# Optimization experiments

Measured on AMD Instinct MI355X. Metric: run time of the kernel, lower is better.

The kernel has to match this reference:

```python
import jax, jax.numpy as jnp
import numpy as np

N = 50000      # nodes
E = 800000     # edges (avg degree 16)
IN, HID, OUT = 256, 128, 64


def _glorot(key, shape):
    fan_in, fan_out = shape[0], shape[1]
    limit = np.sqrt(6.0 / (fan_in + fan_out))
    return jax.random.uniform(key, shape, jnp.float32, -limit, limit)


def setup_inputs() -> dict:
    key = jax.random.key(0)
    ks = jax.random.split(key, 8)
    x = jax.random.normal(ks[0], (N, IN), jnp.float32)
    edge_index = jax.random.randint(ks[1], (2, E), 0, N, dtype=jnp.int64)
    W1 = _glorot(ks[2], (IN, HID))
    b1 = jnp.zeros((HID,), jnp.float32)
    W2 = _glorot(ks[3], (HID, OUT))
    b2 = jnp.zeros((OUT,), jnp.float32)
    aw1 = _glorot(ks[4], (HID, 1))
    ab1 = jnp.zeros((1,), jnp.float32)
    aw2 = _glorot(ks[5], (OUT, 1))
    ab2 = jnp.zeros((1,), jnp.float32)
    return {"x": x, "edge_index": edge_index, "W1": W1, "b1": b1,
            "W2": W2, "b2": b2, "aw1": aw1, "ab1": ab1, "aw2": aw2, "ab2": ab2}


def gcn_conv(x, W, b, src, dst, n):
    # PyG GCNConv: add self-loops, symmetric degree normalization, then aggregate.
    h = x @ W                                   # [n, out]
    loops = jnp.arange(n, dtype=src.dtype)
    s = jnp.concatenate([src, loops])           # [E+n]
    d = jnp.concatenate([dst, loops])
    deg = jax.ops.segment_sum(jnp.ones(s.shape[0], h.dtype), d, num_segments=n)
    dinv = jnp.where(deg > 0, jax.lax.rsqrt(deg), 0.0)
    norm = dinv[s] * dinv[d]                    # [E+n]
    out = jax.ops.segment_sum(h[s] * norm[:, None], d, num_segments=n)
    return out + b


def reference(x, edge_index, W1, b1, W2, b2, aw1, ab1, aw2, ab2):
    # eval mode: dropout is identity
    src, dst = edge_index[0], edge_index[1]
    h = gcn_conv(x, W1, b1, src, dst, N)
    h = jax.nn.relu(h)
    h = h * jax.nn.sigmoid(h @ aw1 + ab1)       # sigmoid attention gate 1
    h = gcn_conv(h, W2, b2, src, dst, N)
    return h * jax.nn.sigmoid(h @ aw2 + ab2)    # sigmoid attention gate 2
```

## Files before the change

kernel.cpp:

```cpp
#include <hip/hip_runtime.h>
#include <math.h>

#define N_NODES 50000
#define N_EDGES 800000
#define D_IN    256
#define D_HID   128
#define D_OUT   64

#define NB 196
#define CH 4096

typedef unsigned int u32;
typedef unsigned short u16;
typedef __attribute__((ext_vector_type(8))) short bf16x8;
typedef __attribute__((ext_vector_type(4))) float f32x4;

__device__ __forceinline__ float bflo(u32 u) {
    union { u32 i; float f; } c; c.i = u << 16; return c.f;
}
__device__ __forceinline__ float bfhi(u32 u) {
    union { u32 i; float f; } c; c.i = u & 0xffff0000u; return c.f;
}
__device__ __forceinline__ u32 pack_bf2(float a, float b) {
    union { float f; u32 i; } ca, cb; ca.f = a; cb.f = b;
    u32 ra = (ca.i + 0x7fffu + ((ca.i >> 16) & 1u)) >> 16;
    u32 rb = (cb.i + 0x7fffu + ((cb.i >> 16) & 1u)) & 0xffff0000u;
    return ra | rb;
}
__device__ __forceinline__ u32 bf16_rne(float f) {
    union { float f; u32 i; } c; c.f = f;
    return (c.i + 0x7fffu + ((c.i >> 16) & 1u)) >> 16;
}
__device__ __forceinline__ float bfbits_to_f32(u32 hb) {
    union { u32 i; float f; } c; c.i = hb << 16; return c.f;
}

__global__ void k_detect(const void* __restrict__ ei, int* __restrict__ flag) {
    int t = threadIdx.x;
    int v = ((const int*)ei)[2 * t + 1];
    if (v != 0) atomicOr(flag, 1);
}

__device__ __forceinline__ int edge_at(const void* ei, int is64, int which, int i) {
    if (is64) return (int)((const long long*)ei)[(size_t)which * N_EDGES + i];
    return ((const int*)ei)[which * N_EDGES + i];
}


__global__ __launch_bounds__(256) void k_hist(const void* __restrict__ ei,
                                              const int* __restrict__ flag,
                                              int* __restrict__ bcnt) {
    __shared__ int h[NB];
    int t = threadIdx.x;
    for (int i = t; i < NB; i += 256) h[i] = 0;
    __syncthreads();
    int is64 = (flag[0] == 0);
    for (int i = blockIdx.x * 256 + t; i < N_EDGES; i += gridDim.x * 256) {
        int d = edge_at(ei, is64, 1, i);
        atomicAdd(&h[d >> 8], 1);
    }
    __syncthreads();
    for (int i = t; i < NB; i += 256) if (h[i]) atomicAdd(&bcnt[i], h[i]);
}

__global__ void k_bscan(const int* __restrict__ bcnt, int* __restrict__ bstart,
                        int* __restrict__ bcur) {
    __shared__ int sm[256];
    int t = threadIdx.x;
    int v = (t < NB) ? bcnt[t] : 0;
    sm[t] = v; __syncthreads();
    for (int off = 1; off < 256; off <<= 1) {
        int a = (t >= off) ? sm[t - off] : 0;
        __syncthreads();
        sm[t] += a;
        __syncthreads();
    }
    if (t < NB) { bstart[t] = sm[t] - v; bcur[t] = sm[t] - v; }
}

__global__ __launch_bounds__(256) void k_scatter1(const void* __restrict__ ei,
                                                  const int* __restrict__ flag,
                                                  int* __restrict__ bcur,
                                                  u32* __restrict__ ebuf) {
    __shared__ int h[NB], gbase[NB], lc[NB];
    int t = threadIdx.x;
    for (int i = t; i < NB; i += 256) { h[i] = 0; lc[i] = 0; }
    __syncthreads();
    int is64 = (flag[0] == 0);
    int base = blockIdx.x * CH;

    u32 p[CH / 256];
    #pragma unroll
    for (int j = 0; j < CH / 256; ++j) {
        int i = base + j * 256 + t;
        if (i < N_EDGES) {
            int s = edge_at(ei, is64, 0, i);
            int d = edge_at(ei, is64, 1, i);
            p[j] = (u32)s | ((u32)d << 16);
            atomicAdd(&h[d >> 8], 1);
        }
    }
    __syncthreads();
    for (int i = t; i < NB; i += 256) if (h[i]) gbase[i] = atomicAdd(&bcur[i], h[i]);
    __syncthreads();
    #pragma unroll
    for (int j = 0; j < CH / 256; ++j) {
        int i = base + j * 256 + t;
        if (i < N_EDGES) {
            int b = (int)(p[j] >> 24);
            int lp = atomicAdd(&lc[b], 1);
            ebuf[gbase[b] + lp] = p[j];
        }
    }
}

__global__ __launch_bounds__(256) void k_scatter2(const u32* __restrict__ ebuf,
                                                  const int* __restrict__ bstart,
                                                  const int* __restrict__ bcnt,
                                                  int* __restrict__ rowstart,
                                                  int* __restrict__ cnt,
                                                  float* __restrict__ dinv,
                                                  int* __restrict__ colidx) {
    __shared__ int h2[256], lofs[256], cur[256], sm[256];
    int b = blockIdx.x, t = threadIdx.x;
    int e0 = bstart[b], ne = bcnt[b];
    h2[t] = 0; cur[t] = 0;
    __syncthreads();
    for (int i = t; i < ne; i += 256) {
        u32 p = ebuf[e0 + i];
        atomicAdd(&h2[(p >> 16) & 255], 1);
    }
    __syncthreads();
    int v = h2[t]; sm[t] = v; __syncthreads();
    for (int off = 1; off < 256; off <<= 1) {
        int a = (t >= off) ? sm[t - off] : 0;
        __syncthreads();
        sm[t] += a;
        __syncthreads();
    }
    lofs[t] = sm[t] - v;
    __syncthreads();
    int node = (b << 8) + t;
    if (node < N_NODES) {
        rowstart[node] = e0 + lofs[t];
        cnt[node] = v;
        dinv[node] = rsqrtf(1.0f + (float)v);
    }
    for (int i = t; i < ne; i += 256) {
        u32 p = ebuf[e0 + i];
        int dl = (p >> 16) & 255;
        int lp = atomicAdd(&cur[dl], 1);
        colidx[e0 + lofs[dl] + lp] = (int)(p & 0xffffu);
    }
}

__global__ void k_wsplit(const float* __restrict__ W, u16* __restrict__ tHi,
                         u16* __restrict__ tLo, int K, int NF) {
    int i = blockIdx.x * 256 + threadIdx.x;
    if (i >= K * NF) return;
    int k = i / NF, c = i - k * NF;
    float f = W[i];
    u32 hb = bf16_rne(f);
    u32 lb = bf16_rne(f - bfbits_to_f32(hb));
    tHi[(size_t)c * K + k] = (u16)hb;
    tLo[(size_t)c * K + k] = (u16)lb;
}

template <int K, int NF>
__global__ __launch_bounds__(256) void k_gemm_mfma(
    const float* __restrict__ A, const u16* __restrict__ tHi,
    const u16* __restrict__ tLo, const float* __restrict__ dinv,
    u32* __restrict__ Cp, int M) {
    constexpr int NT = NF / 16;
    constexpr int LDK = 40;
    __shared__ u16 aH[128][LDK], aL[128][LDK];
    __shared__ u16 wH[NF][LDK], wL[NF][LDK];

    const int t = threadIdx.x;
    const int lane = t & 63, wv = t >> 6;
    const int m0 = blockIdx.x * 128;
    const int lr = lane & 15, lk = (lane >> 4) * 8;

    f32x4 acc[2][NT] = {};

    const int arow = t >> 1;
    const int akq = (t & 1) * 16;
    const bool aok = (m0 + arow) < M;
    const float* asrc = A + (size_t)(m0 + arow) * K + akq;

    for (int ks = 0; ks < K; ks += 32) {
        {
            float buf[16];
            #pragma unroll
            for (int j = 0; j < 16; ++j) buf[j] = 0.0f;
            if (aok) {
                const float4* p = (const float4*)(asrc + ks);
                float4 v0 = p[0], v1 = p[1], v2 = p[2], v3 = p[3];
                buf[0] = v0.x; buf[1] = v0.y; buf[2]  = v0.z; buf[3]  = v0.w;
                buf[4] = v1.x; buf[5] = v1.y; buf[6]  = v1.z; buf[7]  = v1.w;
                buf[8] = v2.x; buf[9] = v2.y; buf[10] = v2.z; buf[11] = v2.w;
                buf[12] = v3.x; buf[13] = v3.y; buf[14] = v3.z; buf[15] = v3.w;
            }
            u32 h[16], l[16];
            #pragma unroll
            for (int j = 0; j < 16; ++j) {
                h[j] = bf16_rne(buf[j]);
                l[j] = bf16_rne(buf[j] - bfbits_to_f32(h[j]));
            }
            uint4 hv0 = make_uint4(h[0] | (h[1] << 16), h[2] | (h[3] << 16),
                                   h[4] | (h[5] << 16), h[6] | (h[7] << 16));
            uint4 hv1 = make_uint4(h[8] | (h[9] << 16), h[10] | (h[11] << 16),
                                   h[12] | (h[13] << 16), h[14] | (h[15] << 16));
            uint4 lv0 = make_uint4(l[0] | (l[1] << 16), l[2] | (l[3] << 16),
                                   l[4] | (l[5] << 16), l[6] | (l[7] << 16));
            uint4 lv1 = make_uint4(l[8] | (l[9] << 16), l[10] | (l[11] << 16),
                                   l[12] | (l[13] << 16), l[14] | (l[15] << 16));
            *(uint4*)&aH[arow][akq + 0] = hv0;
            *(uint4*)&aH[arow][akq + 8] = hv1;
            *(uint4*)&aL[arow][akq + 0] = lv0;
            *(uint4*)&aL[arow][akq + 8] = lv1;
        }
        #pragma unroll
        for (int idx = t; idx < NF * 4; idx += 256) {
            int col = idx >> 2;
            int k8 = (idx & 3) * 8;
            *(uint4*)&wH[col][k8] = *(const uint4*)&tHi[(size_t)col * K + ks + k8];
            *(uint4*)&wL[col][k8] = *(const uint4*)&tLo[(size_t)col * K + ks + k8];
        }
        __syncthreads();

        bf16x8 afH[2], afL[2];
        #pragma unroll
        for (int mt = 0; mt < 2; ++mt) {
            int r = wv * 32 + mt * 16 + lr;
            afH[mt] = *(const bf16x8*)&aH[r][lk];
            afL[mt] = *(const bf16x8*)&aL[r][lk];
        }
        #pragma unroll
        for (int nt = 0; nt < NT; ++nt) {
            bf16x8 bh = *(const bf16x8*)&wH[nt * 16 + lr][lk];
            bf16x8 bl = *(const bf16x8*)&wL[nt * 16 + lr][lk];
            #pragma unroll
            for (int mt = 0; mt < 2; ++mt) {
                acc[mt][nt] = __builtin_amdgcn_mfma_f32_16x16x32_bf16(afH[mt], bh, acc[mt][nt], 0, 0, 0);
                acc[mt][nt] = __builtin_amdgcn_mfma_f32_16x16x32_bf16(afL[mt], bh, acc[mt][nt], 0, 0, 0);
                acc[mt][nt] = __builtin_amdgcn_mfma_f32_16x16x32_bf16(afH[mt], bl, acc[mt][nt], 0, 0, 0);
            }
        }
        __syncthreads();
    }

    #pragma unroll
    for (int mt = 0; mt < 2; ++mt) {
        #pragma unroll
        for (int r = 0; r < 4; ++r) {
            int row = m0 + wv * 32 + mt * 16 + (lane >> 4) * 4 + r;
            float dv = (row < M) ? dinv[row] : 0.0f;
            #pragma unroll
            for (int nt = 0; nt < NT; ++nt) {
                float v = acc[mt][nt][r] * dv;
                float vn = __shfl_xor(v, 1);
                if (!(lane & 1) && row < M) {
                    Cp[(size_t)row * (NF / 2) + nt * 8 + (lr >> 1)] = pack_bf2(v, vn);
                }
            }
        }
    }
}


__global__ void k_agg1(const u32* __restrict__ hs, const int* __restrict__ rowstart,
                       const int* __restrict__ cnt, const int* __restrict__ colidx,
                       const float* __restrict__ dinv,
                       const float* __restrict__ b, const float* __restrict__ aw,
                       const float* __restrict__ ab, float* __restrict__ out) {
    int v = blockIdx.x;
    int l = threadIdx.x;
    float dv = dinv[v];
    u32 su = hs[(size_t)v * 64 + l];
    float ax = bflo(su), ay = bfhi(su);
    int start = rowstart[v], len = cnt[v];
    const int* cx = colidx + start;
    int j = 0;
    for (; j + 4 <= len; j += 4) {
        int s0 = cx[j], s1 = cx[j + 1], s2 = cx[j + 2], s3 = cx[j + 3];
        u32 u0 = hs[(size_t)s0 * 64 + l];
        u32 u1 = hs[(size_t)s1 * 64 + l];
        u32 u2 = hs[(size_t)s2 * 64 + l];
        u32 u3 = hs[(size_t)s3 * 64 + l];
        ax += bflo(u0) + bflo(u1) + bflo(u2) + bflo(u3);
        ay += bfhi(u0) + bfhi(u1) + bfhi(u2) + bfhi(u3);
    }
    for (; j < len; ++j) {
        u32 u = hs[(size_t)cx[j] * 64 + l];
        ax += bflo(u); ay += bfhi(u);
    }
    float2 bp = ((const float2*)b)[l];
    ax = fmaxf(ax * dv + bp.x, 0.0f);
    ay = fmaxf(ay * dv + bp.y, 0.0f);
    float2 ap = ((const float2*)aw)[l];
    float p = ax * ap.x + ay * ap.y;
    for (int off = 32; off; off >>= 1) p += __shfl_xor(p, off);
    float g = 1.0f / (1.0f + expf(-(p + ab[0])));
    ((float2*)out)[(size_t)v * 64 + l] = make_float2(ax * g, ay * g);
}

__global__ void k_agg2(const u32* __restrict__ hs, const int* __restrict__ rowstart,
                       const int* __restrict__ cnt, const int* __restrict__ colidx,
                       const float* __restrict__ dinv,
                       const float* __restrict__ b, const float* __restrict__ aw,
                       const float* __restrict__ ab, float* __restrict__ out) {
    int v = blockIdx.x;
    int l = threadIdx.x;
    int c = l & 31, half = l >> 5;
    float dv = dinv[v];
    float ax = 0.0f, ay = 0.0f;
    if (half == 0) {
        u32 su = hs[(size_t)v * 32 + c];
        ax = bflo(su); ay = bfhi(su);
    }
    int start = rowstart[v], len = cnt[v];
    const int* cx = colidx + start;
    int j = half;
    for (; j + 2 < len; j += 4) {
        int s0 = cx[j], s1 = cx[j + 2];
        u32 u0 = hs[(size_t)s0 * 32 + c];
        u32 u1 = hs[(size_t)s1 * 32 + c];
        ax += bflo(u0) + bflo(u1);
        ay += bfhi(u0) + bfhi(u1);
    }
    if (j < len) {
        u32 u = hs[(size_t)cx[j] * 32 + c];
        ax += bflo(u); ay += bfhi(u);
    }
    ax += __shfl_xor(ax, 32);
    ay += __shfl_xor(ay, 32);
    float2 bp = ((const float2*)b)[c];
    ax = ax * dv + bp.x;
    ay = ay * dv + bp.y;
    float2 ap = ((const float2*)aw)[c];
    float p = ax * ap.x + ay * ap.y;
    for (int off = 16; off; off >>= 1) p += __shfl_xor(p, off);
    float g = 1.0f / (1.0f + expf(-(p + ab[0])));
    if (half == 0) ((float2*)out)[(size_t)v * 32 + c] = make_float2(ax * g, ay * g);
}


static inline size_t align_up(size_t x, size_t a) { return (x + a - 1) & ~(a - 1); }

extern "C" void kernel_launch(void* const* d_in, const int* in_sizes, int n_in,
                              void* d_out, int out_size, void* d_ws, size_t ws_size,
                              hipStream_t stream) {
    const float* x   = (const float*)d_in[0];
    const void*  ei  = d_in[1];
    const float* W1  = (const float*)d_in[2];
    const float* b1  = (const float*)d_in[3];
    const float* W2  = (const float*)d_in[4];
    const float* b2  = (const float*)d_in[5];
    const float* aw1 = (const float*)d_in[6];
    const float* ab1 = (const float*)d_in[7];
    const float* aw2 = (const float*)d_in[8];
    const float* ab2 = (const float*)d_in[9];
    float* out = (float*)d_out;

    char* w = (char*)d_ws;
    size_t off = 0;
    int*   flag     = (int*)(w + off); off = align_up(off + 4, 256);
    int*   bcnt     = (int*)(w + off); off = align_up(off + NB * 4, 256);
    int*   bstart   = (int*)(w + off); off = align_up(off + NB * 4, 256);
    int*   bcur     = (int*)(w + off); off = align_up(off + NB * 4, 256);
    int*   cnt      = (int*)(w + off); off = align_up(off + N_NODES * 4, 256);
    int*   rowstart = (int*)(w + off); off = align_up(off + N_NODES * 4, 256);
    float* dinv     = (float*)(w + off); off = align_up(off + N_NODES * 4, 256);
    u32*   ebuf     = (u32*)(w + off); off = align_up(off + (size_t)N_EDGES * 4, 256);
    int*   colidx   = (int*)(w + off); off = align_up(off + (size_t)N_EDGES * 4, 256);
    u32*   h1s      = (u32*)(w + off); off = align_up(off + (size_t)N_NODES * 64 * 4, 256);
    float* h1g      = (float*)(w + off); off = align_up(off + (size_t)N_NODES * D_HID * 4, 256);
    u32*   h2s      = (u32*)(w + off); off = align_up(off + (size_t)N_NODES * 32 * 4, 256);
    u16*   wt1h     = (u16*)(w + off); off = align_up(off + (size_t)D_IN * D_HID * 2, 256);
    u16*   wt1l     = (u16*)(w + off); off = align_up(off + (size_t)D_IN * D_HID * 2, 256);
    u16*   wt2h     = (u16*)(w + off); off = align_up(off + (size_t)D_HID * D_OUT * 2, 256);
    u16*   wt2l     = (u16*)(w + off); off = align_up(off + (size_t)D_HID * D_OUT * 2, 256);
    (void)ws_size; (void)out_size; (void)n_in; (void)in_sizes;

    hipMemsetAsync(flag, 0, 4, stream);
    hipMemsetAsync(bcnt, 0, NB * 4, stream);

    k_detect<<<1, 256, 0, stream>>>(ei, flag);
    k_wsplit<<<(D_IN * D_HID + 255) / 256, 256, 0, stream>>>(W1, wt1h, wt1l, D_IN, D_HID);
    k_wsplit<<<(D_HID * D_OUT + 255) / 256, 256, 0, stream>>>(W2, wt2h, wt2l, D_HID, D_OUT);

    k_hist<<<256, 256, 0, stream>>>(ei, flag, bcnt);
    k_bscan<<<1, 256, 0, stream>>>(bcnt, bstart, bcur);
    k_scatter1<<<(N_EDGES + CH - 1) / CH, 256, 0, stream>>>(ei, flag, bcur, ebuf);
    k_scatter2<<<NB, 256, 0, stream>>>(ebuf, bstart, bcnt, rowstart, cnt, dinv, colidx);

    k_gemm_mfma<D_IN, D_HID><<<(N_NODES + 127) / 128, 256, 0, stream>>>(x, wt1h, wt1l, dinv, h1s, N_NODES);
    k_agg1<<<N_NODES, 64, 0, stream>>>(h1s, rowstart, cnt, colidx, dinv, b1, aw1, ab1, h1g);

    k_gemm_mfma<D_HID, D_OUT><<<(N_NODES + 127) / 128, 256, 0, stream>>>(h1g, wt2h, wt2l, dinv, h2s, N_NODES);
    k_agg2<<<N_NODES, 64, 0, stream>>>(h2s, rowstart, cnt, colidx, dinv, b2, aw2, ab2, out);
}
```

Measured before the change: 246.6 us.

## Fold dtype detection into kernels, merge weight splits, pack four nodes per block

Drops the separate int32/int64 detection kernel and its memset; k_hist and k_scatter1 now each detect the edge dtype themselves in shared memory. The two weight-split launches become one kernel. The aggregation kernels now handle four nodes per 256-thread block instead of one node per 64-thread block, and their gather loops are unrolled deeper to keep more loads in flight. The goals are fewer launches, less block scheduling overhead and better latency hiding, at the cost of redundant detection reads in every block and higher register use.

```diff
diff --git a/kernel.cpp b/kernel.cpp
--- a/kernel.cpp
+++ b/kernel.cpp
@@ -35,26 +35,31 @@
     union { u32 i; float f; } c; c.i = hb << 16; return c.f;
 }
 
-__global__ void k_detect(const void* __restrict__ ei, int* __restrict__ flag) {
-    int t = threadIdx.x;
-    int v = ((const int*)ei)[2 * t + 1];
-    if (v != 0) atomicOr(flag, 1);
-}
-
 __device__ __forceinline__ int edge_at(const void* ei, int is64, int which, int i) {
     if (is64) return (int)((const long long*)ei)[(size_t)which * N_EDGES + i];
     return ((const int*)ei)[which * N_EDGES + i];
 }
 
+__device__ __forceinline__ int detect_is64(const void* ei, int t, int* s_is32) {
+    if (t == 0) *s_is32 = 0;
+    __syncthreads();
+    if (t < 256) {
+        int vv = ((const int*)ei)[2 * t + 1];
+        if (vv != 0) atomicOr(s_is32, 1);
+    }
+    __syncthreads();
+    return (*s_is32 == 0);
+}
+
 
 __global__ __launch_bounds__(256) void k_hist(const void* __restrict__ ei,
-                                              const int* __restrict__ flag,
                                               int* __restrict__ bcnt) {
     __shared__ int h[NB];
+    __shared__ int s_is32;
     int t = threadIdx.x;
+    int is64 = detect_is64(ei, t, &s_is32);
     for (int i = t; i < NB; i += 256) h[i] = 0;
     __syncthreads();
-    int is64 = (flag[0] == 0);
     for (int i = blockIdx.x * 256 + t; i < N_EDGES; i += gridDim.x * 256) {
         int d = edge_at(ei, is64, 1, i);
         atomicAdd(&h[d >> 8], 1);
@@ -79,14 +84,14 @@
 }
 
 __global__ __launch_bounds__(256) void k_scatter1(const void* __restrict__ ei,
-                                                  const int* __restrict__ flag,
                                                   int* __restrict__ bcur,
                                                   u32* __restrict__ ebuf) {
     __shared__ int h[NB], gbase[NB], lc[NB];
+    __shared__ int s_is32;
     int t = threadIdx.x;
+    int is64 = detect_is64(ei, t, &s_is32);
     for (int i = t; i < NB; i += 256) { h[i] = 0; lc[i] = 0; }
     __syncthreads();
-    int is64 = (flag[0] == 0);
     int base = blockIdx.x * CH;
 
     u32 p[CH / 256];
@@ -154,16 +159,27 @@
     }
 }
 
-__global__ void k_wsplit(const float* __restrict__ W, u16* __restrict__ tHi,
-                         u16* __restrict__ tLo, int K, int NF) {
+__global__ void k_wsplit(const float* __restrict__ W1, u16* __restrict__ t1h,
+                         u16* __restrict__ t1l, const float* __restrict__ W2,
+                         u16* __restrict__ t2h, u16* __restrict__ t2l) {
     int i = blockIdx.x * 256 + threadIdx.x;
-    if (i >= K * NF) return;
-    int k = i / NF, c = i - k * NF;
-    float f = W[i];
-    u32 hb = bf16_rne(f);
-    u32 lb = bf16_rne(f - bfbits_to_f32(hb));
-    tHi[(size_t)c * K + k] = (u16)hb;
-    tLo[(size_t)c * K + k] = (u16)lb;
+    if (i < D_IN * D_HID) {
+        int k = i / D_HID, c = i - k * D_HID;
+        float f = W1[i];
+        u32 hb = bf16_rne(f);
+        u32 lb = bf16_rne(f - bfbits_to_f32(hb));
+        t1h[(size_t)c * D_IN + k] = (u16)hb;
+        t1l[(size_t)c * D_IN + k] = (u16)lb;
+    }
+    int j = i - D_IN * D_HID;
+    if (j >= 0 && j < D_HID * D_OUT) {
+        int k = j / D_OUT, c = j - k * D_OUT;
+        float f = W2[j];
+        u32 hb = bf16_rne(f);
+        u32 lb = bf16_rne(f - bfbits_to_f32(hb));
+        t2h[(size_t)c * D_HID + k] = (u16)hb;
+        t2l[(size_t)c * D_HID + k] = (u16)lb;
+    }
 }
 
 template <int K, int NF>
@@ -269,19 +285,37 @@
 }
 
 
-__global__ void k_agg1(const u32* __restrict__ hs, const int* __restrict__ rowstart,
-                       const int* __restrict__ cnt, const int* __restrict__ colidx,
-                       const float* __restrict__ dinv,
-                       const float* __restrict__ b, const float* __restrict__ aw,
-                       const float* __restrict__ ab, float* __restrict__ out) {
-    int v = blockIdx.x;
-    int l = threadIdx.x;
+__global__ __launch_bounds__(256) void k_agg1(
+        const u32* __restrict__ hs, const int* __restrict__ rowstart,
+        const int* __restrict__ cnt, const int* __restrict__ colidx,
+        const float* __restrict__ dinv,
+        const float* __restrict__ b, const float* __restrict__ aw,
+        const float* __restrict__ ab, float* __restrict__ out) {
+    int v = blockIdx.x * 4 + (threadIdx.x >> 6);
+    int l = threadIdx.x & 63;
+    if (v >= N_NODES) return;
     float dv = dinv[v];
     u32 su = hs[(size_t)v * 64 + l];
     float ax = bflo(su), ay = bfhi(su);
     int start = rowstart[v], len = cnt[v];
     const int* cx = colidx + start;
     int j = 0;
+    for (; j + 8 <= len; j += 8) {
+        int s0 = cx[j], s1 = cx[j + 1], s2 = cx[j + 2], s3 = cx[j + 3];
+        int s4 = cx[j + 4], s5 = cx[j + 5], s6 = cx[j + 6], s7 = cx[j + 7];
+        u32 u0 = hs[(size_t)s0 * 64 + l];
+        u32 u1 = hs[(size_t)s1 * 64 + l];
+        u32 u2 = hs[(size_t)s2 * 64 + l];
+        u32 u3 = hs[(size_t)s3 * 64 + l];
+        u32 u4 = hs[(size_t)s4 * 64 + l];
+        u32 u5 = hs[(size_t)s5 * 64 + l];
+        u32 u6 = hs[(size_t)s6 * 64 + l];
+        u32 u7 = hs[(size_t)s7 * 64 + l];
+        ax += bflo(u0) + bflo(u1) + bflo(u2) + bflo(u3)
+            + bflo(u4) + bflo(u5) + bflo(u6) + bflo(u7);
+        ay += bfhi(u0) + bfhi(u1) + bfhi(u2) + bfhi(u3)
+            + bfhi(u4) + bfhi(u5) + bfhi(u6) + bfhi(u7);
+    }
     for (; j + 4 <= len; j += 4) {
         int s0 = cx[j], s1 = cx[j + 1], s2 = cx[j + 2], s3 = cx[j + 3];
         u32 u0 = hs[(size_t)s0 * 64 + l];
@@ -305,13 +339,15 @@
     ((float2*)out)[(size_t)v * 64 + l] = make_float2(ax * g, ay * g);
 }
 
-__global__ void k_agg2(const u32* __restrict__ hs, const int* __restrict__ rowstart,
-                       const int* __restrict__ cnt, const int* __restrict__ colidx,
-                       const float* __restrict__ dinv,
-                       const float* __restrict__ b, const float* __restrict__ aw,
-                       const float* __restrict__ ab, float* __restrict__ out) {
-    int v = blockIdx.x;
-    int l = threadIdx.x;
+__global__ __launch_bounds__(256) void k_agg2(
+        const u32* __restrict__ hs, const int* __restrict__ rowstart,
+        const int* __restrict__ cnt, const int* __restrict__ colidx,
+        const float* __restrict__ dinv,
+        const float* __restrict__ b, const float* __restrict__ aw,
+        const float* __restrict__ ab, float* __restrict__ out) {
+    int v = blockIdx.x * 4 + (threadIdx.x >> 6);
+    int l = threadIdx.x & 63;
+    if (v >= N_NODES) return;
     int c = l & 31, half = l >> 5;
     float dv = dinv[v];
     float ax = 0.0f, ay = 0.0f;
@@ -322,6 +358,15 @@
     int start = rowstart[v], len = cnt[v];
     const int* cx = colidx + start;
     int j = half;
+    for (; j + 6 < len; j += 8) {
+        int s0 = cx[j], s1 = cx[j + 2], s2 = cx[j + 4], s3 = cx[j + 6];
+        u32 u0 = hs[(size_t)s0 * 32 + c];
+        u32 u1 = hs[(size_t)s1 * 32 + c];
+        u32 u2 = hs[(size_t)s2 * 32 + c];
+        u32 u3 = hs[(size_t)s3 * 32 + c];
+        ax += bflo(u0) + bflo(u1) + bflo(u2) + bflo(u3);
+        ay += bfhi(u0) + bfhi(u1) + bfhi(u2) + bfhi(u3);
+    }
     for (; j + 2 < len; j += 4) {
         int s0 = cx[j], s1 = cx[j + 2];
         u32 u0 = hs[(size_t)s0 * 32 + c];
@@ -365,7 +410,6 @@
 
     char* w = (char*)d_ws;
     size_t off = 0;
-    int*   flag     = (int*)(w + off); off = align_up(off + 4, 256);
     int*   bcnt     = (int*)(w + off); off = align_up(off + NB * 4, 256);
     int*   bstart   = (int*)(w + off); off = align_up(off + NB * 4, 256);
     int*   bcur     = (int*)(w + off); off = align_up(off + NB * 4, 256);
@@ -383,21 +427,19 @@
     u16*   wt2l     = (u16*)(w + off); off = align_up(off + (size_t)D_HID * D_OUT * 2, 256);
     (void)ws_size; (void)out_size; (void)n_in; (void)in_sizes;
 
-    hipMemsetAsync(flag, 0, 4, stream);
     hipMemsetAsync(bcnt, 0, NB * 4, stream);
 
-    k_detect<<<1, 256, 0, stream>>>(ei, flag);
-    k_wsplit<<<(D_IN * D_HID + 255) / 256, 256, 0, stream>>>(W1, wt1h, wt1l, D_IN, D_HID);
-    k_wsplit<<<(D_HID * D_OUT + 255) / 256, 256, 0, stream>>>(W2, wt2h, wt2l, D_HID, D_OUT);
-
-    k_hist<<<256, 256, 0, stream>>>(ei, flag, bcnt);
+    k_wsplit<<<(D_IN * D_HID + D_HID * D_OUT + 255) / 256, 256, 0, stream>>>(
+        W1, wt1h, wt1l, W2, wt2h, wt2l);
+
+    k_hist<<<256, 256, 0, stream>>>(ei, bcnt);
     k_bscan<<<1, 256, 0, stream>>>(bcnt, bstart, bcur);
-    k_scatter1<<<(N_EDGES + CH - 1) / CH, 256, 0, stream>>>(ei, flag, bcur, ebuf);
+    k_scatter1<<<(N_EDGES + CH - 1) / CH, 256, 0, stream>>>(ei, bcur, ebuf);
     k_scatter2<<<NB, 256, 0, stream>>>(ebuf, bstart, bcnt, rowstart, cnt, dinv, colidx);
 
     k_gemm_mfma<D_IN, D_HID><<<(N_NODES + 127) / 128, 256, 0, stream>>>(x, wt1h, wt1l, dinv, h1s, N_NODES);
-    k_agg1<<<N_NODES, 64, 0, stream>>>(h1s, rowstart, cnt, colidx, dinv, b1, aw1, ab1, h1g);
+    k_agg1<<<(N_NODES + 3) / 4, 256, 0, stream>>>(h1s, rowstart, cnt, colidx, dinv, b1, aw1, ab1, h1g);
 
     k_gemm_mfma<D_HID, D_OUT><<<(N_NODES + 127) / 128, 256, 0, stream>>>(h1g, wt2h, wt2l, dinv, h2s, N_NODES);
-    k_agg2<<<N_NODES, 64, 0, stream>>>(h2s, rowstart, cnt, colidx, dinv, b2, aw2, ab2, out);
-}
+    k_agg2<<<(N_NODES + 3) / 4, 256, 0, stream>>>(h2s, rowstart, cnt, colidx, dinv, b2, aw2, ab2, out);
+}
```

Measured after the change: 238.0 us. -3.5%, faster.
